# Kernel tuning notes

Measured on AMD Instinct MI355X. Metric: run time of the kernel, lower is better.

The kernel has to match this reference:

```python
import jax, jax.numpy as jnp
import numpy as np

DIM = 192
HEADS = 6
WIN = 64  # 8*8
EPS = 1e-12


def setup_inputs() -> dict:
    key = jax.random.key(0)
    ks = jax.random.split(key, 10)
    s = 0.02
    return {
        "qx": jax.random.normal(ks[0], (8192, WIN, DIM), jnp.float32),
        "kvx": jax.random.normal(ks[1], (4096, WIN, DIM), jnp.float32),
        "pos": jax.random.normal(ks[2], (1, WIN, DIM), jnp.float32) * s,
        "Wq": jax.random.normal(ks[3], (DIM, DIM), jnp.float32) * s,
        "bq": jnp.zeros((DIM,), jnp.float32),
        "Wkv": jax.random.normal(ks[4], (2 * DIM, DIM), jnp.float32) * s,
        "bkv": jnp.zeros((2 * DIM,), jnp.float32),
        "Wp": jax.random.normal(ks[5], (DIM, DIM), jnp.float32) * s,
        "bp": jnp.zeros((DIM,), jnp.float32),
    }


def _l2norm(x):
    # F.normalize: x / max(||x||_2, eps) along last dim
    n = jnp.sqrt(jnp.sum(x * x, axis=-1, keepdims=True))
    return x / jnp.maximum(n, EPS)


def reference(qx, kvx, pos, Wq, bq, Wkv, bkv, Wp, bp):
    B_q, q_len, C = qx.shape
    B_kv, kv_len, _ = kvx.shape
    tile_num = B_q // B_kv
    kvx = jnp.tile(kvx, (tile_num, 1, 1))
    qx = qx + pos
    q = qx @ Wq.T + bq                       # [Bq, q, C]
    kv = kvx @ Wkv.T + bkv                   # [Bq, kv, 2C]
    k, v = kv[..., :C], kv[..., C:]
    hd = C // HEADS
    q = q.reshape(B_q, q_len, HEADS, hd).transpose(0, 2, 1, 3)
    k = k.reshape(B_q, kv_len, HEADS, hd).transpose(0, 2, 1, 3)
    v = v.reshape(B_q, kv_len, HEADS, hd).transpose(0, 2, 1, 3)
    scale = 1.0 / np.sqrt(C).astype(np.float32)
    attn = jnp.einsum("bhqd,bhkd->bhqk", _l2norm(q), _l2norm(k)) * scale
    attn = jax.nn.softmax(attn, axis=-1)
    x = jnp.einsum("bhqk,bhkd->bhqd", attn, v)
    x = x.transpose(0, 2, 1, 3).reshape(B_q, q_len, C)
    return x @ Wp.T + bp
```

## Files before the change

### kernel.cpp

```cpp
#include <hip/hip_runtime.h>
#include <hip/hip_bf16.h>

#define TPB   512
#define CDIM  192
#define LDA   200
#define LDK   200
#define LDVT  72
#define LDST  200
#define VTOFF 12800
#define SCALE 0.07216878364870323f

using short8 = __attribute__((ext_vector_type(8))) short;
using f32x4  = __attribute__((ext_vector_type(4))) float;
using us4    = __attribute__((ext_vector_type(4))) unsigned short;

__device__ __forceinline__ unsigned short hc(float f) {
  __hip_bfloat16 h = __float2bfloat16(f);
  unsigned short u; __builtin_memcpy(&u, &h, 2); return u;
}
__device__ __forceinline__ unsigned pack2(float x, float y) {
  return (unsigned)hc(x) | ((unsigned)hc(y) << 16);
}
__device__ __forceinline__ uint2 packa(f32x4 a) {
  return make_uint2(pack2(a[0], a[1]), pack2(a[2], a[3]));
}
#define MFMA(a, b, c) __builtin_amdgcn_mfma_f32_16x16x32_bf16((a), (b), (c), 0, 0, 0)
#define SCHED_FENCE() __builtin_amdgcn_sched_barrier(0)

#define NWQ  36864
#define NWKV 73728
#define NWP  36864
__global__ void cvt_weights(const float* __restrict__ Wq, const float* __restrict__ Wkv,
                            const float* __restrict__ Wp, unsigned short* __restrict__ o) {
  int i = blockIdx.x * blockDim.x + threadIdx.x;
  if (i < NWQ) o[i] = hc(Wq[i]);
  else if (i < NWQ + NWKV) o[i] = hc(Wkv[i - NWQ]);
  else if (i < NWQ + NWKV + NWP) o[i] = hc(Wp[i - NWQ - NWKV]);
}

__global__ __launch_bounds__(TPB, 4) void wa_v19(
    const float* __restrict__ qx, const float* __restrict__ kvx,
    const float* __restrict__ pos,
    const float* __restrict__ bq, const float* __restrict__ bkv,
    const float* __restrict__ bp,
    const unsigned short* __restrict__ Wqb, const unsigned short* __restrict__ Wkvb,
    const unsigned short* __restrict__ Wpb,
    float* __restrict__ out, int BQ, int BKV)
{
  __shared__ __align__(16) unsigned short sA[64 * LDA];
  __shared__ __align__(16) unsigned short sU[26624];

  const int tid = threadIdx.x;
  const int wid = tid >> 6;
  const int l15 = (tid & 63) & 15;
  const int l4  = (tid & 63) >> 4;

  int g = blockIdx.x;
  int w;
  if (BQ == 2 * BKV && (BKV & 7) == 0) {
    w = ((g >> 4) << 3) + (g & 7) + (((g >> 3) & 1) ? BKV : 0);
  } else {
    w = g;
  }
  const size_t qoff  = (size_t)w * (64 * CDIM);
  const size_t kvoff = (size_t)(w % BKV) * (64 * CDIM);

  const int srcA = l15 + 32 * (l4 & 1);
  const int srcB = srcA + 16;
  const int sel  = l4 >> 1;
  auto redistC = [&](f32x4 cA, f32x4 cB) -> short8 {
    unsigned iA0 = pack2(cA[0], cA[1]), iA1 = pack2(cA[2], cA[3]);
    unsigned iB0 = pack2(cB[0], cB[1]), iB1 = pack2(cB[2], cB[3]);
    unsigned A00 = (unsigned)__shfl((int)iA0, srcA);
    unsigned A01 = (unsigned)__shfl((int)iA1, srcA);
    unsigned A10 = (unsigned)__shfl((int)iB0, srcA);
    unsigned A11 = (unsigned)__shfl((int)iB1, srcA);
    unsigned B00 = (unsigned)__shfl((int)iA0, srcB);
    unsigned B01 = (unsigned)__shfl((int)iA1, srcB);
    unsigned B10 = (unsigned)__shfl((int)iB0, srcB);
    unsigned B11 = (unsigned)__shfl((int)iB1, srcB);
    union { uint4 u; short8 s; } uu;
    uu.u.x = sel ? A10 : A00;
    uu.u.y = sel ? A11 : A01;
    uu.u.z = sel ? B10 : B00;
    uu.u.w = sel ? B11 : B01;
    return uu.s;
  };

  {
    const float4* gq = (const float4*)(qx + qoff);
    const float4* p4 = (const float4*)pos;
    #pragma unroll
    for (int t = 0; t < 6; ++t) {
      int e = tid + t * TPB, row = e / 48, c4 = e % 48;
      float4 a = gq[e], p = p4[e];
      us4 wq;
      wq.x = hc(a.x + p.x); wq.y = hc(a.y + p.y); wq.z = hc(a.z + p.z); wq.w = hc(a.w + p.w);
      *(us4*)&sA[row * LDA + c4 * 4] = wq;
    }
    const float4* gk = (const float4*)(kvx + kvoff);
    #pragma unroll
    for (int t = 0; t < 6; ++t) {
      int e = tid + t * TPB, row = e / 48, c4 = e % 48;
      float4 k = gk[e];
      us4 wk; wk.x = hc(k.x); wk.y = hc(k.y); wk.z = hc(k.z); wk.w = hc(k.w);
      *(us4*)&sU[row * LDST + c4 * 4] = wk;
    }
  }
  __syncthreads();

  auto kproj = [&](int h, short8* kres) {
    f32x4 kacc[4][2];
    #pragma unroll
    for (int mh = 0; mh < 2; ++mh) {
      float4 bk = *(const float4*)&bkv[32 * h + 16 * mh + 4 * l4];
      #pragma unroll
      for (int n = 0; n < 4; ++n) kacc[n][mh] = f32x4{bk.x, bk.y, bk.z, bk.w};
    }
    #pragma unroll
    for (int ks = 0; ks < 6; ++ks) {
      short8 act[4];
      #pragma unroll
      for (int n = 0; n < 4; ++n)
        act[n] = *(const short8*)&sU[(16 * n + l15) * LDST + ks * 32 + 8 * l4];
      #pragma unroll
      for (int mh = 0; mh < 2; ++mh) {
        short8 kw = *(const short8*)&Wkvb[(size_t)(32 * h + 16 * mh + l15) * CDIM + ks * 32 + 8 * l4];
        #pragma unroll
        for (int n = 0; n < 4; ++n) kacc[n][mh] = MFMA(kw, act[n], kacc[n][mh]);
      }
    }
    #pragma unroll
    for (int n = 0; n < 4; ++n) {
      float ss = 0.f;
      #pragma unroll
      for (int mh = 0; mh < 2; ++mh)
        #pragma unroll
        for (int r = 0; r < 4; ++r) ss += kacc[n][mh][r] * kacc[n][mh][r];
      ss += __shfl_xor(ss, 16);
      ss += __shfl_xor(ss, 32);
      float sc = __builtin_amdgcn_rsqf(fmaxf(ss, 1e-24f));
      #pragma unroll
      for (int mh = 0; mh < 2; ++mh)
        #pragma unroll
        for (int r = 0; r < 4; ++r) kacc[n][mh][r] *= sc;
      kres[n] = redistC(kacc[n][0], kacc[n][1]);
    }
  };
  auto vhalf = [&](int h, int nv) {
    f32x4 vacc[4];
    {
      float bv = bkv[CDIM + 32 * h + 16 * nv + l15];
      #pragma unroll
      for (int m = 0; m < 4; ++m) vacc[m] = f32x4{bv, bv, bv, bv};
    }
    #pragma unroll
    for (int ks = 0; ks < 6; ++ks) {
      short8 vw = *(const short8*)&Wkvb[(size_t)(CDIM + 32 * h + 16 * nv + l15) * CDIM + ks * 32 + 8 * l4];
      #pragma unroll
      for (int m = 0; m < 4; ++m) {
        short8 act = *(const short8*)&sU[(16 * m + l15) * LDST + ks * 32 + 8 * l4];
        vacc[m] = MFMA(act, vw, vacc[m]);
      }
    }
    #pragma unroll
    for (int m = 0; m < 4; ++m)
      *(uint2*)&sU[VTOFF + (32 * h + 16 * nv + l15) * LDVT + 16 * m + 4 * l4] = packa(vacc[m]);
  };
  auto qproj = [&](int h, short8* qres) {
    f32x4 qacc[4][2];
    #pragma unroll
    for (int mh = 0; mh < 2; ++mh) {
      float4 bk = *(const float4*)&bq[32 * h + 16 * mh + 4 * l4];
      #pragma unroll
      for (int n = 0; n < 4; ++n) qacc[n][mh] = f32x4{bk.x, bk.y, bk.z, bk.w};
    }
    #pragma unroll
    for (int ks = 0; ks < 6; ++ks) {
      short8 act[4];
      #pragma unroll
      for (int n = 0; n < 4; ++n)
        act[n] = *(const short8*)&sA[(16 * n + l15) * LDA + ks * 32 + 8 * l4];
      #pragma unroll
      for (int mh = 0; mh < 2; ++mh) {
        short8 qw = *(const short8*)&Wqb[(size_t)(32 * h + 16 * mh + l15) * CDIM + ks * 32 + 8 * l4];
        #pragma unroll
        for (int n = 0; n < 4; ++n) qacc[n][mh] = MFMA(qw, act[n], qacc[n][mh]);
      }
    }
    #pragma unroll
    for (int n = 0; n < 4; ++n) {
      float ss = 0.f;
      #pragma unroll
      for (int mh = 0; mh < 2; ++mh)
        #pragma unroll
        for (int r = 0; r < 4; ++r) ss += qacc[n][mh][r] * qacc[n][mh][r];
      ss += __shfl_xor(ss, 16);
      ss += __shfl_xor(ss, 32);
      float sc = SCALE * __builtin_amdgcn_rsqf(fmaxf(ss, 1e-24f));
      #pragma unroll
      for (int mh = 0; mh < 2; ++mh)
        #pragma unroll
        for (int r = 0; r < 4; ++r) qacc[n][mh][r] *= sc;
      qres[n] = redistC(qacc[n][0], qacc[n][1]);
    }
  };

  short8 kres[4];
  const bool hasK = (wid < 6);
  if (hasK) {
    kproj(wid, kres);
    SCHED_FENCE();
    vhalf(wid >> 1, wid & 1);
  } else {
    const int t0 = 6 + (wid - 6) * 3;
    vhalf(t0 >> 1, t0 & 1);
    SCHED_FENCE();
    vhalf((t0 + 1) >> 1, (t0 + 1) & 1);
    SCHED_FENCE();
    vhalf((t0 + 2) >> 1, (t0 + 2) & 1);
  }
  __syncthreads();

  if (hasK) {
    #pragma unroll
    for (int n = 0; n < 4; ++n)
      *(short8*)&sU[(16 * n + l15) * LDK + wid * 32 + 8 * l4] = kres[n];
  }
  SCHED_FENCE();
  short8 qres[4];
  if (wid < 6) qproj(wid, qres);
  __syncthreads();

  if (wid < 6) {
    #pragma unroll
    for (int n = 0; n < 4; ++n)
      *(short8*)&sA[(16 * n + l15) * LDA + wid * 32 + 8 * l4] = qres[n];
  }
  __syncthreads();

  {
    const int t  = wid & 3;
    const int h0 = 3 * (wid >> 2);
    #pragma unroll
    for (int i = 0; i < 3; ++i) {
      const int hh = h0 + i;
      short8 qb = *(const short8*)&sA[(16 * t + l15) * LDA + hh * 32 + 8 * l4];
      f32x4 c[4];
      #pragma unroll
      for (int n = 0; n < 4; ++n) {
        short8 ak = *(const short8*)&sU[(16 * n + l15) * LDK + hh * 32 + 8 * l4];
        f32x4 z = f32x4{0.f, 0.f, 0.f, 0.f};
        c[n] = MFMA(ak, qb, z);
      }
      float sum = 0.f;
      #pragma unroll
      for (int n = 0; n < 4; ++n)
        #pragma unroll
        for (int r = 0; r < 4; ++r) { c[n][r] = __expf(c[n][r]); sum += c[n][r]; }
      sum += __shfl_xor(sum, 16);
      sum += __shfl_xor(sum, 32);
      const float inv = __builtin_amdgcn_rcpf(sum);
      #pragma unroll
      for (int n = 0; n < 4; ++n)
        #pragma unroll
        for (int r = 0; r < 4; ++r) c[n][r] *= inv;
      short8 pa0 = redistC(c[0], c[1]);
      short8 pa1 = redistC(c[2], c[3]);
      f32x4 cx0 = f32x4{0.f, 0.f, 0.f, 0.f};
      f32x4 cx1 = f32x4{0.f, 0.f, 0.f, 0.f};
      {
        short8 av00 = *(const short8*)&sU[VTOFF + (hh * 32 + l15) * LDVT + 8 * l4];
        short8 av01 = *(const short8*)&sU[VTOFF + (hh * 32 + l15) * LDVT + 32 + 8 * l4];
        cx0 = MFMA(av00, pa0, cx0);
        cx0 = MFMA(av01, pa1, cx0);
        short8 av10 = *(const short8*)&sU[VTOFF + (hh * 32 + 16 + l15) * LDVT + 8 * l4];
        short8 av11 = *(const short8*)&sU[VTOFF + (hh * 32 + 16 + l15) * LDVT + 32 + 8 * l4];
        cx1 = MFMA(av10, pa0, cx1);
        cx1 = MFMA(av11, pa1, cx1);
      }
      short8 xf = redistC(cx0, cx1);
      *(short8*)&sA[(16 * t + l15) * LDA + hh * 32 + 8 * l4] = xf;
    }
  }
  __syncthreads();

  {
    {
      const int n = wid;
      f32x4 oacc[4];
      float bv = bp[n * 16 + l15];
      #pragma unroll
      for (int m = 0; m < 4; ++m) oacc[m] = f32x4{bv, bv, bv, bv};
      #pragma unroll
      for (int ks = 0; ks < 6; ++ks) {
        short8 pw = *(const short8*)&Wpb[(size_t)(n * 16 + l15) * CDIM + ks * 32 + 8 * l4];
        #pragma unroll
        for (int m = 0; m < 4; ++m) {
          short8 xa = *(const short8*)&sA[(16 * m + l15) * LDA + ks * 32 + 8 * l4];
          oacc[m] = MFMA(xa, pw, oacc[m]);
        }
      }
      #pragma unroll
      for (int m = 0; m < 4; ++m)
        #pragma unroll
        for (int r = 0; r < 4; ++r)
          out[qoff + (size_t)(16 * m + 4 * l4 + r) * CDIM + n * 16 + l15] = oacc[m][r];
    }
    SCHED_FENCE();
    {
      const int n = 8 + (wid >> 1);
      const int m0 = 2 * (wid & 1);
      f32x4 oacc[2];
      float bv = bp[n * 16 + l15];
      oacc[0] = f32x4{bv, bv, bv, bv};
      oacc[1] = f32x4{bv, bv, bv, bv};
      #pragma unroll
      for (int ks = 0; ks < 6; ++ks) {
        short8 pw = *(const short8*)&Wpb[(size_t)(n * 16 + l15) * CDIM + ks * 32 + 8 * l4];
        #pragma unroll
        for (int mm = 0; mm < 2; ++mm) {
          short8 xa = *(const short8*)&sA[(16 * (m0 + mm) + l15) * LDA + ks * 32 + 8 * l4];
          oacc[mm] = MFMA(xa, pw, oacc[mm]);
        }
      }
      #pragma unroll
      for (int mm = 0; mm < 2; ++mm)
        #pragma unroll
        for (int r = 0; r < 4; ++r)
          out[qoff + (size_t)(16 * (m0 + mm) + 4 * l4 + r) * CDIM + n * 16 + l15] = oacc[mm][r];
    }
  }
}

extern "C" void kernel_launch(void* const* d_in, const int* in_sizes, int n_in,
                              void* d_out, int out_size, void* d_ws, size_t ws_size,
                              hipStream_t stream) {
  const float* qx  = (const float*)d_in[0];
  const float* kvx = (const float*)d_in[1];
  const float* pos = (const float*)d_in[2];
  const float* Wq  = (const float*)d_in[3];
  const float* bq  = (const float*)d_in[4];
  const float* Wkv = (const float*)d_in[5];
  const float* bkv = (const float*)d_in[6];
  const float* Wp  = (const float*)d_in[7];
  const float* bp  = (const float*)d_in[8];
  float* out = (float*)d_out;
  unsigned short* wsb = (unsigned short*)d_ws;

  const int BQ  = in_sizes[0] / (64 * CDIM);
  const int BKV = in_sizes[1] / (64 * CDIM);

  const int ncvt = NWQ + NWKV + NWP;
  cvt_weights<<<(ncvt + 255) / 256, 256, 0, stream>>>(Wq, Wkv, Wp, wsb);

  wa_v19<<<BQ, TPB, 0, stream>>>(qx, kvx, pos, bq, bkv, bp,
                                 wsb, wsb + NWQ, wsb + NWQ + NWKV, out, BQ, BKV);
}
```

Measured before the change: 468.7 us.

## Rebalance K/V/Q projection work across waves and drop one block barrier

Splits the V projection into quarter tiles (2 row-blocks each) instead of half tiles. Waves 0-5 now do K projection, one V quarter and the Q projection back-to-back, while waves 6-7 each do nine V quarters. This lets Q projection overlap with the V work of the other waves and removes one __syncthreads phase. The risk is that the extra register pressure from holding kres and qres together in the head waves, or an uneven per-wave load, could lengthen the critical path.

```diff
diff --git a/kernel.cpp b/kernel.cpp
--- a/kernel.cpp
+++ b/kernel.cpp
@@ -38,7 +38,7 @@
   else if (i < NWQ + NWKV + NWP) o[i] = hc(Wp[i - NWQ - NWKV]);
 }
 
-__global__ __launch_bounds__(TPB, 4) void wa_v19(
+__global__ __launch_bounds__(TPB, 4) void wa_v20(
     const float* __restrict__ qx, const float* __restrict__ kvx,
     const float* __restrict__ pos,
     const float* __restrict__ bq, const float* __restrict__ bkv,
@@ -147,25 +147,25 @@
       kres[n] = redistC(kacc[n][0], kacc[n][1]);
     }
   };
-  auto vhalf = [&](int h, int nv) {
-    f32x4 vacc[4];
+  auto vquarter = [&](int h, int nv, int mp) {
+    f32x4 vacc[2];
     {
       float bv = bkv[CDIM + 32 * h + 16 * nv + l15];
-      #pragma unroll
-      for (int m = 0; m < 4; ++m) vacc[m] = f32x4{bv, bv, bv, bv};
+      vacc[0] = f32x4{bv, bv, bv, bv};
+      vacc[1] = f32x4{bv, bv, bv, bv};
     }
     #pragma unroll
     for (int ks = 0; ks < 6; ++ks) {
       short8 vw = *(const short8*)&Wkvb[(size_t)(CDIM + 32 * h + 16 * nv + l15) * CDIM + ks * 32 + 8 * l4];
       #pragma unroll
-      for (int m = 0; m < 4; ++m) {
-        short8 act = *(const short8*)&sU[(16 * m + l15) * LDST + ks * 32 + 8 * l4];
-        vacc[m] = MFMA(act, vw, vacc[m]);
-      }
-    }
-    #pragma unroll
-    for (int m = 0; m < 4; ++m)
-      *(uint2*)&sU[VTOFF + (32 * h + 16 * nv + l15) * LDVT + 16 * m + 4 * l4] = packa(vacc[m]);
+      for (int mm = 0; mm < 2; ++mm) {
+        short8 act = *(const short8*)&sU[(16 * (2 * mp + mm) + l15) * LDST + ks * 32 + 8 * l4];
+        vacc[mm] = MFMA(act, vw, vacc[mm]);
+      }
+    }
+    #pragma unroll
+    for (int mm = 0; mm < 2; ++mm)
+      *(uint2*)&sU[VTOFF + (32 * h + 16 * nv + l15) * LDVT + 16 * (2 * mp + mm) + 4 * l4] = packa(vacc[mm]);
   };
   auto qproj = [&](int h, short8* qres) {
     f32x4 qacc[4][2];
@@ -206,33 +206,28 @@
     }
   };
 
-  short8 kres[4];
-  const bool hasK = (wid < 6);
-  if (hasK) {
+  short8 kres[4], qres[4];
+  const bool isHead = (wid < 6);
+  if (isHead) {
     kproj(wid, kres);
     SCHED_FENCE();
-    vhalf(wid >> 1, wid & 1);
+    vquarter(wid >> 2, (wid >> 1) & 1, wid & 1);
+    SCHED_FENCE();
+    qproj(wid, qres);
   } else {
-    const int t0 = 6 + (wid - 6) * 3;
-    vhalf(t0 >> 1, t0 & 1);
-    SCHED_FENCE();
-    vhalf((t0 + 1) >> 1, (t0 + 1) & 1);
-    SCHED_FENCE();
-    vhalf((t0 + 2) >> 1, (t0 + 2) & 1);
+    #pragma unroll
+    for (int j = 0; j < 9; ++j) {
+      int qi = 6 + (wid - 6) * 9 + j;
+      vquarter(qi >> 2, (qi >> 1) & 1, qi & 1);
+      SCHED_FENCE();
+    }
   }
   __syncthreads();
 
-  if (hasK) {
+  if (isHead) {
     #pragma unroll
     for (int n = 0; n < 4; ++n)
       *(short8*)&sU[(16 * n + l15) * LDK + wid * 32 + 8 * l4] = kres[n];
-  }
-  SCHED_FENCE();
-  short8 qres[4];
-  if (wid < 6) qproj(wid, qres);
-  __syncthreads();
-
-  if (wid < 6) {
     #pragma unroll
     for (int n = 0; n < 4; ++n)
       *(short8*)&sA[(16 * n + l15) * LDA + wid * 32 + 8 * l4] = qres[n];
@@ -354,6 +349,6 @@
   const int ncvt = NWQ + NWKV + NWP;
   cvt_weights<<<(ncvt + 255) / 256, 256, 0, stream>>>(Wq, Wkv, Wp, wsb);
 
-  wa_v19<<<BQ, TPB, 0, stream>>>(qx, kvx, pos, bq, bkv, bp,
+  wa_v20<<<BQ, TPB, 0, stream>>>(qx, kvx, pos, bq, bkv, bp,
                                  wsb, wsb + NWQ, wsb + NWQ + NWKV, out, BQ, BKV);
 }
```

After: 537.1 us. 14.6% more time.
